# Kernel optimization log

Hardware: AMD Instinct MI355X
Metric: run time of the kernel (lower is better)

Reference implementation:

```python
import jax, jax.numpy as jnp
import numpy as np

D_MODEL = 1024
N_HEADS = 16
D_K = D_MODEL // N_HEADS
THETA = 10000.0
SEQ = 2048
BATCH = 2


def setup_inputs() -> dict:
    key = jax.random.key(0)
    ks = jax.random.split(key, 5)
    std = (2.0 / (D_MODEL + D_MODEL)) ** 0.5
    return {
        "x": jax.random.normal(ks[0], (BATCH, SEQ, D_MODEL), dtype=jnp.float32),
        "token_positions": jnp.arange(SEQ, dtype=jnp.int64 if jax.config.jax_enable_x64 else jnp.int32),
        "wq": jax.random.normal(ks[1], (D_MODEL, D_MODEL), dtype=jnp.float32) * std,
        "wk": jax.random.normal(ks[2], (D_MODEL, D_MODEL), dtype=jnp.float32) * std,
        "wv": jax.random.normal(ks[3], (D_MODEL, D_MODEL), dtype=jnp.float32) * std,
        "wo": jax.random.normal(ks[4], (D_MODEL, D_MODEL), dtype=jnp.float32) * std,
    }


def _apply_rope(t, token_positions):
    # t: [b, h, s, d_k]; interleaved even/odd rotation (RoPE)
    k = jnp.arange(D_K // 2, dtype=t.dtype)
    inv_freq = THETA ** (-2.0 * k / D_K)                     # [d_k/2]
    angles = token_positions.astype(t.dtype)[:, None] * inv_freq  # [s, d_k/2]
    cos, sin = jnp.cos(angles), jnp.sin(angles)
    even, odd = t[..., 0::2], t[..., 1::2]
    re = even * cos - odd * sin
    ro = odd * cos + even * sin
    # re-interleave: stack last then reshape back to [..., d_k]
    return jnp.stack([re, ro], axis=-1).reshape(t.shape)


def reference(x, token_positions, wq, wk, wv, wo):
    b, s, _ = x.shape
    def proj(w):
        y = jnp.einsum("bsd,ed->bse", x, w)               # Linear: x @ W^T
        return y.reshape(b, s, N_HEADS, D_K).transpose(0, 2, 1, 3)  # [b,h,s,dk]
    q, k, v = proj(wq), proj(wk), proj(wv)
    q = _apply_rope(q, token_positions)
    k = _apply_rope(k, token_positions)
    scores = jnp.einsum("bhqd,bhkd->bhqk", q, k) / jnp.sqrt(jnp.asarray(D_K, x.dtype))
    attn = jax.nn.softmax(scores, axis=-1)
    out = jnp.einsum("bhqk,bhkd->bhqd", attn, v)          # [b,h,s,dk]
    out = out.transpose(0, 2, 1, 3).reshape(b, s, D_MODEL)
    return jnp.einsum("bsd,ed->bse", out, wo)
```

## Files before the change

kernel.cpp:

```cpp
#include <hip/hip_runtime.h>
#include <stdint.h>

typedef __bf16 bf16x8 __attribute__((ext_vector_type(8)));
typedef __bf16 bf16x2 __attribute__((ext_vector_type(2)));
typedef float f32x4 __attribute__((ext_vector_type(4)));
typedef float f32x16 __attribute__((ext_vector_type(16)));
typedef unsigned short ushort_t;
typedef unsigned int uint;

#define SEQ    2048
#define DMODEL 1024
#define NHEAD  16
#define DKH    64
#define NBATCH 2
#define MROWS  (NBATCH*SEQ)
#define LOG2E  1.44269504088896340736f

__device__ __forceinline__ uint pk2(float a, float b) {
  bf16x2 t; t[0] = (__bf16)a; t[1] = (__bf16)b;
  return __builtin_bit_cast(uint, t);
}
__device__ __forceinline__ ushort_t b1(float a) {
  return __builtin_bit_cast(ushort_t, (__bf16)a);
}
__device__ __forceinline__ float fexp2(float x) {
#if __has_builtin(__builtin_amdgcn_exp2f)
  return __builtin_amdgcn_exp2f(x);
#else
  return exp2f(x);
#endif
}

__device__ __forceinline__ void gload16(const void* g, void* l) {
  __builtin_amdgcn_global_load_lds(
      (const __attribute__((address_space(1))) void*)g,
      (__attribute__((address_space(3))) void*)l, 16, 0, 0);
}

__device__ __forceinline__ f32x4 mfma16(bf16x8 a, bf16x8 b, f32x4 c) {
  return __builtin_amdgcn_mfma_f32_16x16x32_bf16(a, b, c, 0, 0, 0);
}
__device__ __forceinline__ f32x16 mfma32(bf16x8 a, bf16x8 b, f32x16 c) {
  return __builtin_amdgcn_mfma_f32_32x32x16_bf16(a, b, c, 0, 0, 0);
}

__global__ __launch_bounds__(256) void cvt_all(
    const float* __restrict__ x, const float* __restrict__ wq,
    const float* __restrict__ wk, const float* __restrict__ wv,
    const float* __restrict__ wo, uint2* __restrict__ out)
{
  int b = blockIdx.x;
  const float4* src; uint2* dst; int i;
  if (b < 4096) {
    i = b * 256 + threadIdx.x; src = (const float4*)x; dst = out;
  } else {
    int s = (b - 4096) >> 10;
    i = ((b - 4096) & 1023) * 256 + threadIdx.x;
    src = (const float4*)(s == 0 ? wq : s == 1 ? wk : s == 2 ? wv : wo);
    dst = out + (size_t)1048576 + (size_t)s * 262144;
  }
  float4 v = src[i];
  uint2 r; r.x = pk2(v.x, v.y); r.y = pk2(v.z, v.w);
  dst[i] = r;
}

__global__ __launch_bounds__(256) void rope_tab_kernel(const int* __restrict__ tokpos, float2* __restrict__ tab) {
  int t = blockIdx.x * 256 + threadIdx.x;
  int s = t >> 5, k = t & 31;
  double inv = pow(10000.0, -(double)(2 * k) / 64.0);
  double ang = (double)tokpos[s] * inv;
  tab[t] = make_float2((float)cos(ang), (float)sin(ang));
}

__global__ __launch_bounds__(256) void gemm_nt(
    const ushort_t* __restrict__ A, const ushort_t* __restrict__ W,
    const float2* __restrict__ tab,
    ushort_t* __restrict__ Qo, ushort_t* __restrict__ Ko, ushort_t* __restrict__ Vo,
    float* __restrict__ outf, int fused)
{
  __shared__ ushort_t lA[2][128 * 64];
  __shared__ ushort_t lB[2][128 * 64];
  const int tid = threadIdx.x;
  const int w = tid >> 6, l = tid & 63, lo = l & 15, hi = l >> 4;
  const int wr = (w >> 1) * 64, wc = (w & 1) * 64;
  const char* Ab = (const char*)A + (size_t)blockIdx.y * 128 * 2048;
  const char* Bb = (const char*)W + (size_t)blockIdx.x * 128 * 2048;
  f32x4 acc[4][4] = {};

  const int o0 = w * 1024 + l * 16;
  const int r0 = o0 >> 7;
  const int us = ((o0 >> 4) & 7) ^ (r0 & 7);
  const char* ap = Ab + (size_t)r0 * 2048 + us * 16;
  const char* bp = Bb + (size_t)r0 * 2048 + us * 16;

  auto stage = [&](char* dA, char* dB, const char* aq, const char* bq) {
    #pragma unroll
    for (int i = 0; i < 4; ++i) {
      gload16(aq + i * 65536, dA + w * 1024 + i * 4096);
      gload16(bq + i * 65536, dB + w * 1024 + i * 4096);
    }
  };
  auto comp = [&](const ushort_t* lAb, const ushort_t* lBb) {
    #pragma unroll
    for (int c = 0; c < 2; ++c) {
      bf16x8 af[4], wf[4];
      #pragma unroll
      for (int m = 0; m < 4; ++m) {
        int row = wr + m * 16 + lo;
        af[m] = *(const bf16x8*)((const char*)lAb + row * 128 + ((c * 64 + hi * 16) ^ ((row & 7) << 4)));
      }
      #pragma unroll
      for (int n = 0; n < 4; ++n) {
        int row = wc + n * 16 + lo;
        wf[n] = *(const bf16x8*)((const char*)lBb + row * 128 + ((c * 64 + hi * 16) ^ ((row & 7) << 4)));
      }
      #pragma unroll
      for (int m = 0; m < 4; ++m)
        #pragma unroll
        for (int n = 0; n < 4; ++n)
          acc[m][n] = mfma16(af[m], wf[n], acc[m][n]);
    }
  };

  stage((char*)lA[0], (char*)lB[0], ap, bp); ap += 128; bp += 128;
  __syncthreads();
  for (int it = 0; it < 16; it += 2) {
    stage((char*)lA[1], (char*)lB[1], ap, bp); ap += 128; bp += 128;
    comp(lA[0], lB[0]);
    __syncthreads();
    if (it + 2 < 16) { stage((char*)lA[0], (char*)lB[0], ap, bp); ap += 128; bp += 128; }
    comp(lA[1], lB[1]);
    __syncthreads();
  }

  const int mode = fused ? (blockIdx.x >> 3) : 3;
  const int colblk = fused ? (blockIdx.x & 7) : blockIdx.x;
  const int rowbase = blockIdx.y * 128 + wr + hi * 4;
  const int colbase = colblk * 128 + wc + lo;

  if (mode == 3) {
    #pragma unroll
    for (int m = 0; m < 4; ++m)
      #pragma unroll
      for (int n = 0; n < 4; ++n) {
        int e = colbase + n * 16;
        #pragma unroll
        for (int r = 0; r < 4; ++r) {
          int row = rowbase + m * 16 + r;
          outf[(size_t)row * 1024 + e] = acc[m][n][r];
        }
      }
    return;
  }
  if (mode == 2) {
    #pragma unroll
    for (int m = 0; m < 4; ++m) {
      int row0 = rowbase + m * 16;
      int b = row0 >> 11, s = row0 & 2047;
      #pragma unroll
      for (int n = 0; n < 4; ++n) {
        int e = colbase + n * 16;
        int h = e >> 6, dk = e & 63;
        uint2 pk;
        pk.x = pk2(acc[m][n][0], acc[m][n][1]);
        pk.y = pk2(acc[m][n][2], acc[m][n][3]);
        *(uint2*)(Vo + ((size_t)((b * NHEAD + h) * DKH + dk) * SEQ + s)) = pk;
      }
    }
    return;
  }
  ushort_t* outb = (mode == 0) ? Qo : Ko;
  const float qscale = (mode == 0) ? (0.125f * LOG2E) : 1.0f;
  #pragma unroll
  for (int m = 0; m < 4; ++m) {
    #pragma unroll
    for (int n = 0; n < 4; ++n) {
      int e = colbase + n * 16;
      int h = e >> 6, dk = e & 63, kf = dk >> 1;
      float sgn = (e & 1) ? 1.0f : -1.0f;
      #pragma unroll
      for (int r = 0; r < 4; ++r) {
        int row = rowbase + m * 16 + r;
        int s = row & 2047, b = row >> 11;
        float2 cs = tab[s * 32 + kf];
        float v = acc[m][n][r];
        float p = __shfl_xor(v, 1, 64);
        float res = (v * cs.x + sgn * p * cs.y) * qscale;
        outb[((size_t)((b * NHEAD + h) * SEQ + s)) * DKH + dk] = b1(res);
      }
    }
  }
}

__global__ __launch_bounds__(256) void attn_fwd(
    const ushort_t* __restrict__ Qg, const ushort_t* __restrict__ Kg,
    const ushort_t* __restrict__ VTg, ushort_t* __restrict__ attn)
{
  __shared__ char lds[81920];
  const int tid = threadIdx.x;
  const int w = tid >> 6, l = tid & 63;
  const int qh = w >> 1, kp = w & 1;
  const int q31 = l & 31, hf = l >> 5, s7 = l & 7;
  const int bh = blockIdx.y;
  const int q0 = blockIdx.x * 128 + qh * 64;
  const char* Kb = (const char*)Kg + (size_t)bh * 2048 * 128;
  const char* Vb = (const char*)VTg + (size_t)bh * 64 * 4096;

  bf16x8 qreg[2][4];
  #pragma unroll
  for (int qb = 0; qb < 2; ++qb) {
    const ushort_t* qp = Qg + ((size_t)bh * 2048 + q0 + qb * 32 + q31) * 64 + hf * 8;
    #pragma unroll
    for (int c = 0; c < 4; ++c) qreg[qb][c] = *(const bf16x8*)(qp + c * 16);
  }

  f32x16 accO[2][2] = {};
  float lsum[2] = {0.f, 0.f};

  const char* ra[4];
  #pragma unroll
  for (int c = 0; c < 4; ++c)
    ra[c] = lds + q31 * 128 + ((c * 32 + hf * 16) ^ (s7 << 4));
  const int lP = 49152 + w * 8192;
  char* wb = lds + lP + q31 * 128 + hf * 8;
  const int bq = kp * 8192;

  const int srow = tid >> 3, sw = (tid & 7) * 16;
  const int wl = sw ^ ((srow & 7) << 4);
  const char* ksp = Kb + (size_t)srow * 128 + wl;
  const char* vsp = Vb + (size_t)(srow + ((wl >> 6) & 1) * 32) * 4096 + (wl & 63);

  auto stageT = [&](int slot) {
    gload16(ksp,        lds + slot + tid * 16);
    gload16(ksp + 4096, lds + slot + 8192 + tid * 16);
    gload16(vsp,        lds + slot + 4096 + tid * 16);
    gload16(vsp + 64,   lds + slot + 12288 + tid * 16);
    ksp += 8192; vsp += 128;
  };

  auto tileC = [&](int slot) {
    const int bo = slot + bq;
    bf16x8 kf[4];
    #pragma unroll
    for (int c = 0; c < 4; ++c)
      kf[c] = *(const bf16x8*)(ra[c] + bo);
    f32x16 s0 = {}, s1 = {};
    #pragma unroll
    for (int c = 0; c < 4; ++c) {
      s0 = mfma32(kf[c], qreg[0][c], s0);
      s1 = mfma32(kf[c], qreg[1][c], s1);
    }
    float p0[16], p1[16];
    float t0 = 0.f, t1 = 0.f;
    #pragma unroll
    for (int r = 0; r < 16; ++r) { p0[r] = fexp2(s0[r]); t0 += p0[r]; }
    #pragma unroll
    for (int r = 0; r < 16; ++r) { p1[r] = fexp2(s1[r]); t1 += p1[r]; }
    lsum[0] += t0; lsum[1] += t1;
    #pragma unroll
    for (int g2 = 0; g2 < 4; ++g2) {
      uint2 pk;
      pk.x = pk2(p0[g2 * 4 + 0], p0[g2 * 4 + 1]);
      pk.y = pk2(p0[g2 * 4 + 2], p0[g2 * 4 + 3]);
      *(uint2*)(wb + ((g2 * 16) ^ (s7 << 4))) = pk;
    }
    #pragma unroll
    for (int g2 = 0; g2 < 4; ++g2) {
      uint2 pk;
      pk.x = pk2(p1[g2 * 4 + 0], p1[g2 * 4 + 1]);
      pk.y = pk2(p1[g2 * 4 + 2], p1[g2 * 4 + 3]);
      *(uint2*)(wb + 4096 + ((g2 * 16) ^ (s7 << 4))) = pk;
    }
    #pragma unroll
    for (int kcl = 0; kcl < 2; ++kcl) {
      bf16x8 pb0 = *(const bf16x8*)(ra[kcl] + lP);
      bf16x8 pb1 = *(const bf16x8*)(ra[kcl] + lP + 4096);
      bf16x8 vf0 = *(const bf16x8*)(ra[kcl]     + bo + 4096);
      bf16x8 vf1 = *(const bf16x8*)(ra[kcl + 2] + bo + 4096);
      accO[0][0] = mfma32(vf0, pb0, accO[0][0]);
      accO[0][1] = mfma32(vf1, pb0, accO[0][1]);
      accO[1][0] = mfma32(vf0, pb1, accO[1][0]);
      accO[1][1] = mfma32(vf1, pb1, accO[1][1]);
    }
  };

  stageT(0);
  stageT(16384);
  #pragma unroll 1
  for (int it = 0; it < 10; ++it) {
    #pragma unroll
    for (int j = 0; j < 3; ++j) {
      asm volatile("s_waitcnt vmcnt(4)" ::: "memory");
      __builtin_amdgcn_s_barrier();
      __builtin_amdgcn_sched_barrier(0);
      stageT(((j + 2) % 3) * 16384);
      tileC(j * 16384);
    }
  }
  asm volatile("s_waitcnt vmcnt(4)" ::: "memory");
  __builtin_amdgcn_s_barrier();
  __builtin_amdgcn_sched_barrier(0);
  tileC(0);
  asm volatile("s_waitcnt vmcnt(0)" ::: "memory");
  __builtin_amdgcn_s_barrier();
  __builtin_amdgcn_sched_barrier(0);
  tileC(16384);

  __syncthreads();
  if (kp) {
    char* dst = lds + qh * 16384;
    #pragma unroll
    for (int qb = 0; qb < 2; ++qb)
      #pragma unroll
      for (int db = 0; db < 2; ++db)
        #pragma unroll
        for (int c2 = 0; c2 < 4; ++c2) {
          int j = qb * 8 + db * 4 + c2;
          f32x4 v = { accO[qb][db][c2 * 4 + 0], accO[qb][db][c2 * 4 + 1],
                      accO[qb][db][c2 * 4 + 2], accO[qb][db][c2 * 4 + 3] };
          *(f32x4*)(dst + j * 1024 + l * 16) = v;
        }
    *(float2*)(lds + 32768 + qh * 512 + l * 8) = make_float2(lsum[0], lsum[1]);
  }
  __syncthreads();
  if (!kp) {
    const char* srcp = lds + qh * 16384;
    #pragma unroll
    for (int qb = 0; qb < 2; ++qb)
      #pragma unroll
      for (int db = 0; db < 2; ++db)
        #pragma unroll
        for (int c2 = 0; c2 < 4; ++c2) {
          int j = qb * 8 + db * 4 + c2;
          f32x4 v = *(const f32x4*)(srcp + j * 1024 + l * 16);
          accO[qb][db][c2 * 4 + 0] += v[0];
          accO[qb][db][c2 * 4 + 1] += v[1];
          accO[qb][db][c2 * 4 + 2] += v[2];
          accO[qb][db][c2 * 4 + 3] += v[3];
        }
    float2 lo = *(const float2*)(lds + 32768 + qh * 512 + l * 8);
    lsum[0] += lo.x; lsum[1] += lo.y;

    int b = bh >> 4, head = bh & 15;
    #pragma unroll
    for (int qb = 0; qb < 2; ++qb) {
      float lt = lsum[qb] + __shfl_xor(lsum[qb], 32, 64);
      float inv = 1.0f / lt;
      ushort_t* op = attn + (size_t)(b * 2048 + q0 + qb * 32 + q31) * 1024 + head * 64;
      #pragma unroll
      for (int db = 0; db < 2; ++db)
        #pragma unroll
        for (int m = 0; m < 4; ++m) {
          int d0 = db * 32 + m * 8 + hf * 4;
          uint2 pk;
          pk.x = pk2(accO[qb][db][m * 4 + 0] * inv, accO[qb][db][m * 4 + 1] * inv);
          pk.y = pk2(accO[qb][db][m * 4 + 2] * inv, accO[qb][db][m * 4 + 3] * inv);
          *(uint2*)(op + d0) = pk;
        }
    }
  }
}

extern "C" void kernel_launch(void* const* d_in, const int* in_sizes, int n_in,
                              void* d_out, int out_size, void* d_ws, size_t ws_size,
                              hipStream_t stream) {
  const float* x  = (const float*)d_in[0];
  const int* tok  = (const int*)d_in[1];
  const float* wq = (const float*)d_in[2];
  const float* wk = (const float*)d_in[3];
  const float* wv = (const float*)d_in[4];
  const float* wo = (const float*)d_in[5];
  float* out = (float*)d_out;
  char* ws = (char*)d_ws;

  size_t off = 0;
  float2* tab = (float2*)(ws + off); off += (size_t)SEQ * 32 * sizeof(float2);
  ushort_t* xb  = (ushort_t*)(ws + off); off += (size_t)MROWS * DMODEL * 2;
  ushort_t* wqkv = (ushort_t*)(ws + off); off += (size_t)3 * DMODEL * DMODEL * 2;
  ushort_t* wob = (ushort_t*)(ws + off); off += (size_t)DMODEL * DMODEL * 2;
  ushort_t* Qg  = (ushort_t*)(ws + off); off += (size_t)MROWS * DMODEL * 2;
  ushort_t* Kg  = (ushort_t*)(ws + off); off += (size_t)MROWS * DMODEL * 2;
  ushort_t* VTg = (ushort_t*)(ws + off); off += (size_t)MROWS * DMODEL * 2;
  ushort_t* attnb = xb;
  if (ws_size < off) return;

  cvt_all<<<8192, 256, 0, stream>>>(x, wq, wk, wv, wo, (uint2*)xb);
  rope_tab_kernel<<<256, 256, 0, stream>>>(tok, tab);

  gemm_nt<<<dim3(24, 32), 256, 0, stream>>>(xb, wqkv, tab, Qg, Kg, VTg, nullptr, 1);

  attn_fwd<<<dim3(SEQ / 128, NBATCH * NHEAD), 256, 0, stream>>>(Qg, Kg, VTg, attnb);

  gemm_nt<<<dim3(8, 32), 256, 0, stream>>>(attnb, wob, nullptr, nullptr, nullptr, nullptr, out, 0);
}
```

Baseline: 129.5 us.

## Feed softmax probabilities to PV MFMA directly from registers via permuted V layout

The V projection epilogue now writes V^T with a permuted sequence index so that the accumulator layout of the QK^T MFMA output matches the B-operand layout needed by the PV MFMA. This lets the attention kernel pack exp'd scores into bf16 registers and use them directly, removing the LDS round trip for P and shrinking shared memory from 80KB to 48KB. The cost is a coupled layout dependency between the projection and attention kernels, where any mismatch would silently corrupt results.

```diff
diff --git a/kernel.cpp b/kernel.cpp
--- a/kernel.cpp
+++ b/kernel.cpp
@@ -7,6 +7,7 @@
 typedef float f32x16 __attribute__((ext_vector_type(16)));
 typedef unsigned short ushort_t;
 typedef unsigned int uint;
+typedef uint uint4v __attribute__((ext_vector_type(4)));
 
 #define SEQ    2048
 #define DMODEL 1024
@@ -157,6 +158,8 @@
     for (int m = 0; m < 4; ++m) {
       int row0 = rowbase + m * 16;
       int b = row0 >> 11, s = row0 & 2047;
+      int b2 = (s >> 2) & 3;
+      int sp = (s & ~12) | ((b2 & 1) << 3) | ((b2 >> 1) << 2);
       #pragma unroll
       for (int n = 0; n < 4; ++n) {
         int e = colbase + n * 16;
@@ -164,7 +167,7 @@
         uint2 pk;
         pk.x = pk2(acc[m][n][0], acc[m][n][1]);
         pk.y = pk2(acc[m][n][2], acc[m][n][3]);
-        *(uint2*)(Vo + ((size_t)((b * NHEAD + h) * DKH + dk) * SEQ + s)) = pk;
+        *(uint2*)(Vo + ((size_t)((b * NHEAD + h) * DKH + dk) * SEQ + sp)) = pk;
       }
     }
     return;
@@ -196,7 +199,7 @@
     const ushort_t* __restrict__ Qg, const ushort_t* __restrict__ Kg,
     const ushort_t* __restrict__ VTg, ushort_t* __restrict__ attn)
 {
-  __shared__ char lds[81920];
+  __shared__ char lds[49152];
   const int tid = threadIdx.x;
   const int w = tid >> 6, l = tid & 63;
   const int qh = w >> 1, kp = w & 1;
@@ -221,8 +224,6 @@
   #pragma unroll
   for (int c = 0; c < 4; ++c)
     ra[c] = lds + q31 * 128 + ((c * 32 + hf * 16) ^ (s7 << 4));
-  const int lP = 49152 + w * 8192;
-  char* wb = lds + lP + q31 * 128 + hf * 8;
   const int bq = kp * 8192;
 
   const int srow = tid >> 3, sw = (tid & 7) * 16;
@@ -258,23 +259,15 @@
     for (int r = 0; r < 16; ++r) { p1[r] = fexp2(s1[r]); t1 += p1[r]; }
     lsum[0] += t0; lsum[1] += t1;
     #pragma unroll
-    for (int g2 = 0; g2 < 4; ++g2) {
-      uint2 pk;
-      pk.x = pk2(p0[g2 * 4 + 0], p0[g2 * 4 + 1]);
-      pk.y = pk2(p0[g2 * 4 + 2], p0[g2 * 4 + 3]);
-      *(uint2*)(wb + ((g2 * 16) ^ (s7 << 4))) = pk;
-    }
-    #pragma unroll
-    for (int g2 = 0; g2 < 4; ++g2) {
-      uint2 pk;
-      pk.x = pk2(p1[g2 * 4 + 0], p1[g2 * 4 + 1]);
-      pk.y = pk2(p1[g2 * 4 + 2], p1[g2 * 4 + 3]);
-      *(uint2*)(wb + 4096 + ((g2 * 16) ^ (s7 << 4))) = pk;
-    }
-    #pragma unroll
     for (int kcl = 0; kcl < 2; ++kcl) {
-      bf16x8 pb0 = *(const bf16x8*)(ra[kcl] + lP);
-      bf16x8 pb1 = *(const bf16x8*)(ra[kcl] + lP + 4096);
+      const float* a0 = p0 + kcl * 8;
+      const float* a1 = p1 + kcl * 8;
+      uint4v u0 = { pk2(a0[0], a0[1]), pk2(a0[2], a0[3]),
+                    pk2(a0[4], a0[5]), pk2(a0[6], a0[7]) };
+      uint4v u1 = { pk2(a1[0], a1[1]), pk2(a1[2], a1[3]),
+                    pk2(a1[4], a1[5]), pk2(a1[6], a1[7]) };
+      bf16x8 pb0 = __builtin_bit_cast(bf16x8, u0);
+      bf16x8 pb1 = __builtin_bit_cast(bf16x8, u1);
       bf16x8 vf0 = *(const bf16x8*)(ra[kcl]     + bo + 4096);
       bf16x8 vf1 = *(const bf16x8*)(ra[kcl + 2] + bo + 4096);
       accO[0][0] = mfma32(vf0, pb0, accO[0][0]);
```

Result: no change. 129.7 us (+0.2%).
